# Optimization experiments

Measured on AMD Instinct MI355X. Metric: run time of the kernel, lower is better.

## Reference

```python
import jax, jax.numpy as jnp
import numpy as np

N = 50000      # nodes
E = 800000     # edges (avg degree 16)
F_IN = 128     # num_node_features
D = 64         # embedding_size (= per-head out_channels)
H = 4          # heads
ED = 20        # edge_dim (hardcoded in module)
SLOPE = 0.2    # GATv2 leaky_relu negative slope
N_LAYERS = 3   # conv applied 3 times with shared weights


def setup_inputs() -> dict:
    key = jax.random.key(0)
    ks = jax.random.split(key, 12)
    s = 0.1
    return {
        "x": jax.random.normal(ks[0], (N, F_IN), jnp.float32),
        "edge_attr": jax.random.normal(ks[1], (E, 2), jnp.float32),
        "edge_index": jax.random.randint(ks[2], (2, E), 0, N, dtype=jnp.int32),
        # f: Linear(F_IN, D)
        "f_W": jax.random.normal(ks[3], (F_IN, D), jnp.float32) * s,
        "f_b": jnp.zeros((D,), jnp.float32),
        # fe: Linear(2, ED)
        "fe_W": jax.random.normal(ks[4], (2, ED), jnp.float32) * s,
        "fe_b": jnp.zeros((ED,), jnp.float32),
        # GATv2Conv lin_l / lin_r: Linear(D, H*D)
        "Wl": jax.random.normal(ks[5], (D, H * D), jnp.float32) * s,
        "bl": jnp.zeros((H * D,), jnp.float32),
        "Wr": jax.random.normal(ks[6], (D, H * D), jnp.float32) * s,
        "br": jnp.zeros((H * D,), jnp.float32),
        # lin_edge: Linear(ED, H*D, bias=False)
        "We": jax.random.normal(ks[7], (ED, H * D), jnp.float32) * s,
        # attention vector att: [H, D]
        "att": jax.random.normal(ks[8], (H, D), jnp.float32) * s,
        # final bias (concat=False -> size D)
        "bias": jnp.zeros((D,), jnp.float32),
    }


def _gatv2_conv(h, e_emb, src, dst, Wl, bl, Wr, br, We, att, bias):
    # h: [N, D], e_emb: [E, ED], src/dst: [E]
    xl = (h @ Wl + bl).reshape(-1, H, D)        # source transform  [N,H,D]
    xr = (h @ Wr + br).reshape(-1, H, D)        # target transform  [N,H,D]
    ee = (e_emb @ We).reshape(-1, H, D)         # edge transform    [E,H,D]
    m = jax.nn.leaky_relu(xl[src] + xr[dst] + ee, SLOPE)  # [E,H,D]
    score = jnp.einsum('ehd,hd->eh', m, att)    # [E,H]
    # segment softmax over incoming edges of each dst node
    smax = jax.ops.segment_max(score, dst, num_segments=N)   # [N,H]
    ex = jnp.exp(score - smax[dst])
    denom = jax.ops.segment_sum(ex, dst, num_segments=N)     # [N,H]
    alpha = ex / denom[dst]                                  # [E,H]
    out = jax.ops.segment_sum(alpha[:, :, None] * xl[src], dst, num_segments=N)  # [N,H,D]
    return out.mean(axis=1) + bias              # concat=False -> head mean, [N,D]


def reference(x, edge_attr, edge_index, f_W, f_b, fe_W, fe_b, Wl, bl, Wr, br, We, att, bias):
    src, dst = edge_index[0], edge_index[1]
    h = jax.nn.relu(x @ f_W + f_b)
    e = jax.nn.relu(edge_attr @ fe_W + fe_b)
    for _ in range(N_LAYERS):
        h = jax.nn.relu(_gatv2_conv(h, e, src, dst, Wl, bl, Wr, br, We, att, bias))
    return h
```

## Files before the change

kernel.cpp:

```cpp
#include <hip/hip_runtime.h>
#include <math.h>

#define LN2_INV 1.4426950408889634f

__device__ __forceinline__ float fexp2(float x) {
#if __has_builtin(__builtin_amdgcn_exp2f)
    return __builtin_amdgcn_exp2f(x);
#else
    return exp2f(x);
#endif
}

__device__ __forceinline__ int rdlane_i(int v, int k) {
    return __builtin_amdgcn_readlane(v, k);
}

#define DPP_ADD4(P, CTRL)                                                                   \
    P.x += __int_as_float(__builtin_amdgcn_update_dpp(0, __float_as_int(P.x), CTRL, 0xf, 0xf, true)); \
    P.y += __int_as_float(__builtin_amdgcn_update_dpp(0, __float_as_int(P.y), CTRL, 0xf, 0xf, true)); \
    P.z += __int_as_float(__builtin_amdgcn_update_dpp(0, __float_as_int(P.z), CTRL, 0xf, 0xf, true)); \
    P.w += __int_as_float(__builtin_amdgcn_update_dpp(0, __float_as_int(P.w), CTRL, 0xf, 0xf, true));

__device__ __forceinline__ float4 wave_sum4(float4 p) {
    DPP_ADD4(p, 0x111)
    DPP_ADD4(p, 0x112)
    DPP_ADD4(p, 0x114)
    DPP_ADD4(p, 0x118)
    DPP_ADD4(p, 0x142)
    DPP_ADD4(p, 0x143)
    float4 r;
    r.x = __int_as_float(rdlane_i(__float_as_int(p.x), 63));
    r.y = __int_as_float(rdlane_i(__float_as_int(p.y), 63));
    r.z = __int_as_float(rdlane_i(__float_as_int(p.z), 63));
    r.w = __int_as_float(rdlane_i(__float_as_int(p.w), 63));
    return r;
}

__global__ void k_prep(const float* __restrict__ Wl, const float* __restrict__ Wr,
                       const float* __restrict__ We, const float* __restrict__ att,
                       float* __restrict__ Wlp, float* __restrict__ Wrp,
                       float* __restrict__ Wep, float* __restrict__ attp) {
    int t = blockIdx.x * 256 + threadIdx.x;
    if (t < 64 * 256) {
        int k = t >> 8, c = t & 255;
        int h = c >> 6, d = c & 63;
        int cp = d * 4 + h;
        Wlp[k * 256 + cp] = Wl[t];
        Wrp[k * 256 + cp] = Wr[t];
        if (k < 20) Wep[k * 256 + cp] = We[t];
        if (k == 0) {
            attp[cp] = att[c] * LN2_INV;
            attp[256 + cp] = 0.2f * att[c] * LN2_INV;
        }
    }
}

__global__ __launch_bounds__(256) void k_h0(const float* __restrict__ x,
                                            const float* __restrict__ fW,
                                            const float* __restrict__ fb,
                                            float* __restrict__ h0) {
    __shared__ __align__(16) float xs[8 * 128];
    int t = threadIdx.x;
    int base = blockIdx.x * 8;
#pragma unroll
    for (int r = 0; r < 4; ++r) { int j = r * 256 + t; xs[j] = x[base * 128 + j]; }
    __syncthreads();
    int c = t & 63, half = t >> 6;
    float acc0 = fb[c], acc1 = fb[c];
    int m0 = half, m1 = half + 4;
#pragma unroll 8
    for (int k0 = 0; k0 < 128; k0 += 4) {
        float4 a = *(const float4*)&xs[m0 * 128 + k0];
        float4 b = *(const float4*)&xs[m1 * 128 + k0];
        float w0 = fW[(k0 + 0) * 64 + c], w1 = fW[(k0 + 1) * 64 + c];
        float w2 = fW[(k0 + 2) * 64 + c], w3 = fW[(k0 + 3) * 64 + c];
        acc0 = fmaf(a.x, w0, fmaf(a.y, w1, fmaf(a.z, w2, fmaf(a.w, w3, acc0))));
        acc1 = fmaf(b.x, w0, fmaf(b.y, w1, fmaf(b.z, w2, fmaf(b.w, w3, acc1))));
    }
    h0[(base + m0) * 64 + c] = fmaxf(acc0, 0.f);
    h0[(base + m1) * 64 + c] = fmaxf(acc1, 0.f);
}

__global__ __launch_bounds__(256) void k_xlxr(const float* __restrict__ h,
                                              const float* __restrict__ Wlp,
                                              const float* __restrict__ Wrp,
                                              const float* __restrict__ bl,
                                              const float* __restrict__ br,
                                              float* __restrict__ xl,
                                              float* __restrict__ xr) {
    __shared__ __align__(16) float hs[16 * 64];
    int t = threadIdx.x;
    int base = blockIdx.x * 16;
#pragma unroll
    for (int r = 0; r < 4; ++r) hs[r * 256 + t] = h[base * 64 + r * 256 + t];
    __syncthreads();
    int hh = t & 3, d = t >> 2;
    int co = hh * 64 + d;
    float bL = bl[co], bR = br[co];
    float accl[16], accr[16];
#pragma unroll
    for (int m = 0; m < 16; ++m) { accl[m] = bL; accr[m] = bR; }
#pragma unroll 4
    for (int k0 = 0; k0 < 64; k0 += 4) {
        float wl[4], wr[4];
#pragma unroll
        for (int q = 0; q < 4; ++q) {
            wl[q] = Wlp[(k0 + q) * 256 + t];
            wr[q] = Wrp[(k0 + q) * 256 + t];
        }
#pragma unroll
        for (int m = 0; m < 16; ++m) {
            float4 hv = *(const float4*)&hs[m * 64 + k0];
            accl[m] = fmaf(hv.x, wl[0], fmaf(hv.y, wl[1], fmaf(hv.z, wl[2], fmaf(hv.w, wl[3], accl[m]))));
            accr[m] = fmaf(hv.x, wr[0], fmaf(hv.y, wr[1], fmaf(hv.z, wr[2], fmaf(hv.w, wr[3], accr[m]))));
        }
    }
#pragma unroll
    for (int m = 0; m < 16; ++m) {
        xl[(base + m) * 256 + t] = accl[m];
        xr[(base + m) * 256 + t] = accr[m];
    }
}

__global__ void k_zero(int* __restrict__ deg, int* __restrict__ counter, int Nn) {
    int i = blockIdx.x * 256 + threadIdx.x;
    if (i < Nn) deg[i] = 0;
    if (i == 0) *counter = 0;
}

__global__ void k_count(const int* __restrict__ dstArr, int* __restrict__ deg, int Ee) {
    int e = blockIdx.x * 256 + threadIdx.x;
    if (e < Ee) atomicAdd(&deg[dstArr[e]], 1);
}

__global__ void k_alloc(const int* __restrict__ deg, int* __restrict__ counter,
                        int* __restrict__ start, int* __restrict__ cursor, int Nn) {
    int n = blockIdx.x * 256 + threadIdx.x;
    if (n < Nn) {
        int d = deg[n];
        int b = atomicAdd(counter, d);
        start[n] = b;
        cursor[n] = b;
    }
}

__global__ void k_fill(const int* __restrict__ dstArr, const int* __restrict__ srcArr,
                       const float* __restrict__ eattr, int* __restrict__ cursor,
                       int* __restrict__ rec, int Ee) {
    int e = blockIdx.x * 256 + threadIdx.x;
    if (e < Ee) {
        int p = atomicAdd(&cursor[dstArr[e]], 1);
        int* r = rec + (size_t)p * 32;
        r[0] = srcArr[e];
        r[21] = __float_as_int(eattr[2 * e]);
        r[22] = __float_as_int(eattr[2 * e + 1]);
    }
}

__global__ void k_expand(const float* __restrict__ feW, const float* __restrict__ feb,
                         int* __restrict__ rec, int Ee) {
    int p = blockIdx.x * 8 + (threadIdx.x >> 5);
    int k = threadIdx.x & 31;
    if (p < Ee && k < 20) {
        int* r = rec + (size_t)p * 32;
        float a0 = __int_as_float(r[21]);
        float a1 = __int_as_float(r[22]);
        float s = fmaf(a0, feW[k], fmaf(a1, feW[20 + k], feb[k]));
        r[1 + k] = __float_as_int(fmaxf(s, 0.f));
    }
}

__global__ __launch_bounds__(256, 3) void k_edge(
    const float4* __restrict__ xl4p, const float4* __restrict__ xr4p,
    const float4* __restrict__ attboth, const float4* __restrict__ we4p,
    const int* __restrict__ rec,
    const int* __restrict__ start, const int* __restrict__ deg,
    const float* __restrict__ bias, float* __restrict__ hout, int Nn) {
    int lane = threadIdx.x & 63;
    int n = (int)((blockIdx.x * (unsigned)blockDim.x + threadIdx.x) >> 6);
    if (n >= Nn) return;

    float b = bias[lane];
    int dn = deg[n];
    if (dn == 0) { hout[(size_t)n * 64 + lane] = fmaxf(b, 0.f); return; }
    int s0 = start[n];

    float4 att4  = attboth[lane];
    float4 att02 = attboth[64 + lane];
    float4 xr4 = xr4p[(size_t)n * 64 + lane];
    float4 we[20];
#pragma unroll
    for (int k = 0; k < 20; ++k) we[k] = we4p[k * 64 + lane];

    const int* rp = rec + (size_t)s0 * 32 + (lane & 31);
    int rv0 = rp[0];
    int rv1 = rp[(dn > 1 ? 1 : 0) * 32];
    int src0 = rdlane_i(rv0, 0);
    float4 xl0 = xl4p[(size_t)src0 * 64 + lane];

    float4 acc = make_float4(0.f, 0.f, 0.f, 0.f);
    float4 l   = make_float4(0.f, 0.f, 0.f, 0.f);

    for (int i = 0; i < dn; ++i) {
        int i2 = (i + 2 < dn) ? (i + 2) : (dn - 1);
        int rv2 = rp[i2 * 32];
        int src1 = rdlane_i(rv1, 0);
        float4 xl1 = xl4p[(size_t)src1 * 64 + lane];

        float4 ee = make_float4(0.f, 0.f, 0.f, 0.f);
#pragma unroll
        for (int k = 0; k < 20; ++k) {
            float sk = __int_as_float(rdlane_i(rv0, 1 + k));
            ee.x = fmaf(sk, we[k].x, ee.x);
            ee.y = fmaf(sk, we[k].y, ee.y);
            ee.z = fmaf(sk, we[k].z, ee.z);
            ee.w = fmaf(sk, we[k].w, ee.w);
        }

        float4 p; float v;
        v = xl0.x + xr4.x + ee.x; p.x = fmaf(att4.x, fmaxf(v, 0.f), att02.x * fminf(v, 0.f));
        v = xl0.y + xr4.y + ee.y; p.y = fmaf(att4.y, fmaxf(v, 0.f), att02.y * fminf(v, 0.f));
        v = xl0.z + xr4.z + ee.z; p.z = fmaf(att4.z, fmaxf(v, 0.f), att02.z * fminf(v, 0.f));
        v = xl0.w + xr4.w + ee.w; p.w = fmaf(att4.w, fmaxf(v, 0.f), att02.w * fminf(v, 0.f));

        float4 sc = wave_sum4(p);
        float wx = fexp2(sc.x), wy = fexp2(sc.y), wz = fexp2(sc.z), ww = fexp2(sc.w);
        l.x += wx; l.y += wy; l.z += wz; l.w += ww;
        acc.x = fmaf(wx, xl0.x, acc.x);
        acc.y = fmaf(wy, xl0.y, acc.y);
        acc.z = fmaf(wz, xl0.z, acc.z);
        acc.w = fmaf(ww, xl0.w, acc.w);

        rv0 = rv1; rv1 = rv2; xl0 = xl1;
    }

    float res = 0.25f * (acc.x / l.x + acc.y / l.y + acc.z / l.z + acc.w / l.w) + b;
    hout[(size_t)n * 64 + lane] = fmaxf(res, 0.f);
}

extern "C" void kernel_launch(void* const* d_in, const int* in_sizes, int n_in,
                              void* d_out, int out_size, void* d_ws, size_t ws_size,
                              hipStream_t stream) {
    const float* x     = (const float*)d_in[0];
    const float* eattr = (const float*)d_in[1];
    const int*   eidx  = (const int*)d_in[2];
    const float* fW    = (const float*)d_in[3];
    const float* fb    = (const float*)d_in[4];
    const float* feW   = (const float*)d_in[5];
    const float* feb   = (const float*)d_in[6];
    const float* Wl    = (const float*)d_in[7];
    const float* bl    = (const float*)d_in[8];
    const float* Wr    = (const float*)d_in[9];
    const float* br    = (const float*)d_in[10];
    const float* We    = (const float*)d_in[11];
    const float* att   = (const float*)d_in[12];
    const float* bias  = (const float*)d_in[13];
    float* out = (float*)d_out;

    const int N = in_sizes[0] / 128;
    const int E = in_sizes[1] / 2;
    const int* srcArr = eidx;
    const int* dstArr = eidx + E;

    char* p = (char*)d_ws;
    auto alloc = [&](size_t bytes) -> char* {
        char* r = p;
        p += (bytes + 255) & ~(size_t)255;
        return r;
    };
    float* hA   = (float*)alloc((size_t)N * 64 * 4);
    float* hB   = (float*)alloc((size_t)N * 64 * 4);
    float* xl   = (float*)alloc((size_t)N * 256 * 4);
    float* xr   = (float*)alloc((size_t)N * 256 * 4);
    float* Wlp  = (float*)alloc(64 * 256 * 4);
    float* Wrp  = (float*)alloc(64 * 256 * 4);
    float* Wep  = (float*)alloc(20 * 256 * 4);
    float* attp = (float*)alloc(512 * 4);
    int* deg    = (int*)alloc((size_t)N * 4);
    int* start  = (int*)alloc((size_t)N * 4);
    int* cursor = (int*)alloc((size_t)N * 4);
    int* counter = (int*)alloc(256);
    int* rec    = (int*)alloc((size_t)E * 32 * 4);

    k_prep<<<64, 256, 0, stream>>>(Wl, Wr, We, att, Wlp, Wrp, Wep, attp);
    k_h0<<<N / 8, 256, 0, stream>>>(x, fW, fb, hA);
    k_zero<<<(N + 255) / 256, 256, 0, stream>>>(deg, counter, N);
    k_count<<<(E + 255) / 256, 256, 0, stream>>>(dstArr, deg, E);
    k_alloc<<<(N + 255) / 256, 256, 0, stream>>>(deg, counter, start, cursor, N);
    k_fill<<<(E + 255) / 256, 256, 0, stream>>>(dstArr, srcArr, eattr, cursor, rec, E);
    k_expand<<<(E + 7) / 8, 256, 0, stream>>>(feW, feb, rec, E);

    const float* hin = hA;
    for (int layer = 0; layer < 3; ++layer) {
        float* hout = (layer == 2) ? out : ((layer == 0) ? hB : hA);
        k_xlxr<<<N / 16, 256, 0, stream>>>(hin, Wlp, Wrp, bl, br, xl, xr);
        k_edge<<<(N * 64) / 256, 256, 0, stream>>>(
            (const float4*)xl, (const float4*)xr, (const float4*)attp,
            (const float4*)Wep, rec, start, deg, bias, hout, N);
        hin = hout;
    }
}
```

Before: 1.120 ms.

## Use head-major layout in edge kernel and fuse edge-embedding expansion into fill

Drops the weight permutation kernel and uses the original head-major layout, so each lane holds four d values of one head. The per-edge score reduction becomes a 16-lane DPP row reduction plus one bpermute instead of a full-wave reduction of four values, and the head mean is taken with cross-row shuffles at the end. Edge records shrink from 32 to 24 words, and the edge embedding is computed inside the fill kernel. Each lane now loads the 20 edge features directly with a double-buffered prefetch rather than broadcasting them via readlane. In exchange, every lane issues many more scalar loads per edge, and the math uses packed two-wide vectors.

```diff
diff --git a/kernel.cpp b/kernel.cpp
--- a/kernel.cpp
+++ b/kernel.cpp
@@ -1,5 +1,7 @@
 #include <hip/hip_runtime.h>
 #include <math.h>
+
+typedef float v2f __attribute__((ext_vector_type(2)));
 
 #define LN2_INV 1.4426950408889634f
 
@@ -11,49 +13,15 @@
 #endif
 }
 
-__device__ __forceinline__ int rdlane_i(int v, int k) {
-    return __builtin_amdgcn_readlane(v, k);
-}
-
-#define DPP_ADD4(P, CTRL)                                                                   \
-    P.x += __int_as_float(__builtin_amdgcn_update_dpp(0, __float_as_int(P.x), CTRL, 0xf, 0xf, true)); \
-    P.y += __int_as_float(__builtin_amdgcn_update_dpp(0, __float_as_int(P.y), CTRL, 0xf, 0xf, true)); \
-    P.z += __int_as_float(__builtin_amdgcn_update_dpp(0, __float_as_int(P.z), CTRL, 0xf, 0xf, true)); \
-    P.w += __int_as_float(__builtin_amdgcn_update_dpp(0, __float_as_int(P.w), CTRL, 0xf, 0xf, true));
-
-__device__ __forceinline__ float4 wave_sum4(float4 p) {
-    DPP_ADD4(p, 0x111)
-    DPP_ADD4(p, 0x112)
-    DPP_ADD4(p, 0x114)
-    DPP_ADD4(p, 0x118)
-    DPP_ADD4(p, 0x142)
-    DPP_ADD4(p, 0x143)
-    float4 r;
-    r.x = __int_as_float(rdlane_i(__float_as_int(p.x), 63));
-    r.y = __int_as_float(rdlane_i(__float_as_int(p.y), 63));
-    r.z = __int_as_float(rdlane_i(__float_as_int(p.z), 63));
-    r.w = __int_as_float(rdlane_i(__float_as_int(p.w), 63));
-    return r;
-}
-
-__global__ void k_prep(const float* __restrict__ Wl, const float* __restrict__ Wr,
-                       const float* __restrict__ We, const float* __restrict__ att,
-                       float* __restrict__ Wlp, float* __restrict__ Wrp,
-                       float* __restrict__ Wep, float* __restrict__ attp) {
-    int t = blockIdx.x * 256 + threadIdx.x;
-    if (t < 64 * 256) {
-        int k = t >> 8, c = t & 255;
-        int h = c >> 6, d = c & 63;
-        int cp = d * 4 + h;
-        Wlp[k * 256 + cp] = Wl[t];
-        Wrp[k * 256 + cp] = Wr[t];
-        if (k < 20) Wep[k * 256 + cp] = We[t];
-        if (k == 0) {
-            attp[cp] = att[c] * LN2_INV;
-            attp[256 + cp] = 0.2f * att[c] * LN2_INV;
-        }
-    }
-}
+__device__ __forceinline__ v2f max2(v2f a, float b) {
+    v2f r; r.x = fmaxf(a.x, b); r.y = fmaxf(a.y, b); return r;
+}
+__device__ __forceinline__ v2f min2(v2f a, float b) {
+    v2f r; r.x = fminf(a.x, b); r.y = fminf(a.y, b); return r;
+}
+
+#define DPP_ROW_ADD(V, CTRL) \
+    V += __int_as_float(__builtin_amdgcn_update_dpp(0, __float_as_int(V), CTRL, 0xf, 0xf, true));
 
 __global__ __launch_bounds__(256) void k_h0(const float* __restrict__ x,
                                             const float* __restrict__ fW,
@@ -82,8 +50,8 @@
 }
 
 __global__ __launch_bounds__(256) void k_xlxr(const float* __restrict__ h,
-                                              const float* __restrict__ Wlp,
-                                              const float* __restrict__ Wrp,
+                                              const float* __restrict__ Wl,
+                                              const float* __restrict__ Wr,
                                               const float* __restrict__ bl,
                                               const float* __restrict__ br,
                                               float* __restrict__ xl,
@@ -94,9 +62,7 @@
 #pragma unroll
     for (int r = 0; r < 4; ++r) hs[r * 256 + t] = h[base * 64 + r * 256 + t];
     __syncthreads();
-    int hh = t & 3, d = t >> 2;
-    int co = hh * 64 + d;
-    float bL = bl[co], bR = br[co];
+    float bL = bl[t], bR = br[t];
     float accl[16], accr[16];
 #pragma unroll
     for (int m = 0; m < 16; ++m) { accl[m] = bL; accr[m] = bR; }
@@ -105,8 +71,8 @@
         float wl[4], wr[4];
 #pragma unroll
         for (int q = 0; q < 4; ++q) {
-            wl[q] = Wlp[(k0 + q) * 256 + t];
-            wr[q] = Wrp[(k0 + q) * 256 + t];
+            wl[q] = Wl[(k0 + q) * 256 + t];
+            wr[q] = Wr[(k0 + q) * 256 + t];
         }
 #pragma unroll
         for (int m = 0; m < 16; ++m) {
@@ -145,97 +111,146 @@
 }
 
 __global__ void k_fill(const int* __restrict__ dstArr, const int* __restrict__ srcArr,
-                       const float* __restrict__ eattr, int* __restrict__ cursor,
+                       const float* __restrict__ eattr, const float* __restrict__ feW,
+                       const float* __restrict__ feb, int* __restrict__ cursor,
                        int* __restrict__ rec, int Ee) {
     int e = blockIdx.x * 256 + threadIdx.x;
-    if (e < Ee) {
-        int p = atomicAdd(&cursor[dstArr[e]], 1);
-        int* r = rec + (size_t)p * 32;
-        r[0] = srcArr[e];
-        r[21] = __float_as_int(eattr[2 * e]);
-        r[22] = __float_as_int(eattr[2 * e + 1]);
-    }
-}
-
-__global__ void k_expand(const float* __restrict__ feW, const float* __restrict__ feb,
-                         int* __restrict__ rec, int Ee) {
-    int p = blockIdx.x * 8 + (threadIdx.x >> 5);
-    int k = threadIdx.x & 31;
-    if (p < Ee && k < 20) {
-        int* r = rec + (size_t)p * 32;
-        float a0 = __int_as_float(r[21]);
-        float a1 = __int_as_float(r[22]);
-        float s = fmaf(a0, feW[k], fmaf(a1, feW[20 + k], feb[k]));
-        r[1 + k] = __float_as_int(fmaxf(s, 0.f));
-    }
+    if (e >= Ee) return;
+    float a0 = eattr[2 * e], a1 = eattr[2 * e + 1];
+    int p = atomicAdd(&cursor[dstArr[e]], 1);
+    float* r = (float*)(rec + (size_t)p * 24);
+    float s[20];
+#pragma unroll
+    for (int k = 0; k < 20; ++k)
+        s[k] = fmaxf(fmaf(a0, feW[k], fmaf(a1, feW[20 + k], feb[k])), 0.f);
+#pragma unroll
+    for (int j = 0; j < 5; ++j)
+        ((float4*)r)[j] = make_float4(s[4 * j], s[4 * j + 1], s[4 * j + 2], s[4 * j + 3]);
+    ((int*)r)[20] = srcArr[e];
 }
 
 __global__ __launch_bounds__(256, 3) void k_edge(
     const float4* __restrict__ xl4p, const float4* __restrict__ xr4p,
-    const float4* __restrict__ attboth, const float4* __restrict__ we4p,
-    const int* __restrict__ rec,
-    const int* __restrict__ start, const int* __restrict__ deg,
-    const float* __restrict__ bias, float* __restrict__ hout, int Nn) {
-    int lane = threadIdx.x & 63;
-    int n = (int)((blockIdx.x * (unsigned)blockDim.x + threadIdx.x) >> 6);
+    const float* __restrict__ att, const float4* __restrict__ We4,
+    const int* __restrict__ rec, const int* __restrict__ start,
+    const int* __restrict__ deg, const float* __restrict__ bias,
+    float* __restrict__ hout, int Nn) {
+    const int lane = threadIdx.x & 63;
+    const int n = (int)((blockIdx.x * 256u + threadIdx.x) >> 6);
     if (n >= Nn) return;
 
-    float b = bias[lane];
-    int dn = deg[n];
-    if (dn == 0) { hout[(size_t)n * 64 + lane] = fmaxf(b, 0.f); return; }
-    int s0 = start[n];
-
-    float4 att4  = attboth[lane];
-    float4 att02 = attboth[64 + lane];
-    float4 xr4 = xr4p[(size_t)n * 64 + lane];
-    float4 we[20];
-#pragma unroll
-    for (int k = 0; k < 20; ++k) we[k] = we4p[k * 64 + lane];
-
-    const int* rp = rec + (size_t)s0 * 32 + (lane & 31);
-    int rv0 = rp[0];
-    int rv1 = rp[(dn > 1 ? 1 : 0) * 32];
-    int src0 = rdlane_i(rv0, 0);
-    float4 xl0 = xl4p[(size_t)src0 * 64 + lane];
-
-    float4 acc = make_float4(0.f, 0.f, 0.f, 0.f);
-    float4 l   = make_float4(0.f, 0.f, 0.f, 0.f);
-
-    for (int i = 0; i < dn; ++i) {
-        int i2 = (i + 2 < dn) ? (i + 2) : (dn - 1);
-        int rv2 = rp[i2 * 32];
-        int src1 = rdlane_i(rv1, 0);
-        float4 xl1 = xl4p[(size_t)src1 * 64 + lane];
-
-        float4 ee = make_float4(0.f, 0.f, 0.f, 0.f);
-#pragma unroll
-        for (int k = 0; k < 20; ++k) {
-            float sk = __int_as_float(rdlane_i(rv0, 1 + k));
-            ee.x = fmaf(sk, we[k].x, ee.x);
-            ee.y = fmaf(sk, we[k].y, ee.y);
-            ee.z = fmaf(sk, we[k].z, ee.z);
-            ee.w = fmaf(sk, we[k].w, ee.w);
-        }
-
-        float4 p; float v;
-        v = xl0.x + xr4.x + ee.x; p.x = fmaf(att4.x, fmaxf(v, 0.f), att02.x * fminf(v, 0.f));
-        v = xl0.y + xr4.y + ee.y; p.y = fmaf(att4.y, fmaxf(v, 0.f), att02.y * fminf(v, 0.f));
-        v = xl0.z + xr4.z + ee.z; p.z = fmaf(att4.z, fmaxf(v, 0.f), att02.z * fminf(v, 0.f));
-        v = xl0.w + xr4.w + ee.w; p.w = fmaf(att4.w, fmaxf(v, 0.f), att02.w * fminf(v, 0.f));
-
-        float4 sc = wave_sum4(p);
-        float wx = fexp2(sc.x), wy = fexp2(sc.y), wz = fexp2(sc.z), ww = fexp2(sc.w);
-        l.x += wx; l.y += wy; l.z += wz; l.w += ww;
-        acc.x = fmaf(wx, xl0.x, acc.x);
-        acc.y = fmaf(wy, xl0.y, acc.y);
-        acc.z = fmaf(wz, xl0.z, acc.z);
-        acc.w = fmaf(ww, xl0.w, acc.w);
-
-        rv0 = rv1; rv1 = rv2; xl0 = xl1;
-    }
-
-    float res = 0.25f * (acc.x / l.x + acc.y / l.y + acc.z / l.z + acc.w / l.w) + b;
-    hout[(size_t)n * 64 + lane] = fmaxf(res, 0.f);
+    const int dn = __builtin_amdgcn_readfirstlane(deg[n]);
+    float4 bias4 = ((const float4*)bias)[lane & 15];
+    if (dn == 0) {
+        if (lane < 16) {
+            float4 o = make_float4(fmaxf(bias4.x, 0.f), fmaxf(bias4.y, 0.f),
+                                   fmaxf(bias4.z, 0.f), fmaxf(bias4.w, 0.f));
+            ((float4*)hout)[(size_t)n * 16 + lane] = o;
+        }
+        return;
+    }
+    const int s0 = __builtin_amdgcn_readfirstlane(start[n]);
+    const int* rb = rec + (size_t)s0 * 24;
+
+    float4 attv = ((const float4*)att)[lane];
+    v2f att01 = {attv.x * LN2_INV, attv.y * LN2_INV};
+    v2f att23 = {attv.z * LN2_INV, attv.w * LN2_INV};
+    v2f at201 = 0.2f * att01, at223 = 0.2f * att23;
+    float4 xrv = xr4p[(size_t)n * 64 + lane];
+    v2f xr01 = {xrv.x, xrv.y}, xr23 = {xrv.z, xrv.w};
+    v2f we01[20], we23[20];
+#pragma unroll
+    for (int k = 0; k < 20; ++k) {
+        float4 w = We4[k * 64 + lane];
+        we01[k].x = w.x; we01[k].y = w.y;
+        we23[k].x = w.z; we23[k].y = w.w;
+    }
+    const int bperm = ((lane & 48) | 15) << 2;
+
+    v2f acc01 = {0.f, 0.f}, acc23 = {0.f, 0.f};
+    float l = 0.f;
+
+    float sA[20], sB[20];
+    int src1, src2;
+
+#define LOADS(BUF, IDX)                                                     \
+    {                                                                       \
+        const int* q_ = rb + (size_t)(IDX) * 24;                            \
+        _Pragma("unroll")                                                   \
+        for (int k_ = 0; k_ < 20; ++k_) BUF[k_] = __int_as_float(q_[k_]);   \
+    }
+
+#define PROC(SBUF, XL)                                                      \
+    {                                                                       \
+        v2f xl01 = {XL.x, XL.y}, xl23 = {XL.z, XL.w};                       \
+        v2f ee01 = SBUF[0] * we01[0];                                       \
+        v2f ee23 = SBUF[0] * we23[0];                                       \
+        _Pragma("unroll")                                                   \
+        for (int k_ = 1; k_ < 20; ++k_) {                                   \
+            ee01 += SBUF[k_] * we01[k_];                                    \
+            ee23 += SBUF[k_] * we23[k_];                                    \
+        }                                                                   \
+        v2f v01 = xl01 + xr01 + ee01;                                       \
+        v2f v23 = xl23 + xr23 + ee23;                                       \
+        v2f p01 = att01 * max2(v01, 0.f) + at201 * min2(v01, 0.f);          \
+        v2f p23 = att23 * max2(v23, 0.f) + at223 * min2(v23, 0.f);          \
+        v2f pr = p01 + p23;                                                 \
+        float ps = pr.x + pr.y;                                             \
+        DPP_ROW_ADD(ps, 0x111)                                              \
+        DPP_ROW_ADD(ps, 0x112)                                              \
+        DPP_ROW_ADD(ps, 0x114)                                              \
+        DPP_ROW_ADD(ps, 0x118)                                              \
+        float sc = __int_as_float(                                          \
+            __builtin_amdgcn_ds_bpermute(bperm, __float_as_int(ps)));       \
+        float w_ = fexp2(sc);                                               \
+        l += w_;                                                            \
+        acc01 += w_ * xl01;                                                 \
+        acc23 += w_ * xl23;                                                 \
+    }
+
+    int i1 = dn > 1 ? 1 : 0;
+    LOADS(sA, 0)
+    int srcA0 = rb[20];
+    src1 = rb[(size_t)i1 * 24 + 20];
+    LOADS(sB, i1)
+    float4 xlA = xl4p[(size_t)srcA0 * 64 + lane];
+    float4 xlB;
+
+    int i = 0;
+    while (true) {
+        {
+            int ip2 = i + 2 < dn ? i + 2 : dn - 1;
+            src2 = rb[(size_t)ip2 * 24 + 20];
+            xlB = xl4p[(size_t)src1 * 64 + lane];
+            PROC(sA, xlA)
+            LOADS(sA, ip2)
+            src1 = src2;
+        }
+        if (++i >= dn) break;
+        {
+            int ip2 = i + 2 < dn ? i + 2 : dn - 1;
+            src2 = rb[(size_t)ip2 * 24 + 20];
+            xlA = xl4p[(size_t)src1 * 64 + lane];
+            PROC(sB, xlB)
+            LOADS(sB, ip2)
+            src1 = src2;
+        }
+        if (++i >= dn) break;
+    }
+
+    float inv = 0.25f / l;
+    float4 r = make_float4(acc01.x * inv, acc01.y * inv, acc23.x * inv, acc23.y * inv);
+    r.x += __shfl_xor(r.x, 16, 64); r.x += __shfl_xor(r.x, 32, 64);
+    r.y += __shfl_xor(r.y, 16, 64); r.y += __shfl_xor(r.y, 32, 64);
+    r.z += __shfl_xor(r.z, 16, 64); r.z += __shfl_xor(r.z, 32, 64);
+    r.w += __shfl_xor(r.w, 16, 64); r.w += __shfl_xor(r.w, 32, 64);
+    if (lane < 16) {
+        float4 o = make_float4(fmaxf(r.x + bias4.x, 0.f), fmaxf(r.y + bias4.y, 0.f),
+                               fmaxf(r.z + bias4.z, 0.f), fmaxf(r.w + bias4.w, 0.f));
+        ((float4*)hout)[(size_t)n * 16 + lane] = o;
+    }
+#undef LOADS
+#undef PROC
 }
 
 extern "C" void kernel_launch(void* const* d_in, const int* in_sizes, int n_in,
@@ -272,31 +287,26 @@
     float* hB   = (float*)alloc((size_t)N * 64 * 4);
     float* xl   = (float*)alloc((size_t)N * 256 * 4);
     float* xr   = (float*)alloc((size_t)N * 256 * 4);
-    float* Wlp  = (float*)alloc(64 * 256 * 4);
-    float* Wrp  = (float*)alloc(64 * 256 * 4);
-    float* Wep  = (float*)alloc(20 * 256 * 4);
-    float* attp = (float*)alloc(512 * 4);
     int* deg    = (int*)alloc((size_t)N * 4);
     int* start  = (int*)alloc((size_t)N * 4);
     int* cursor = (int*)alloc((size_t)N * 4);
     int* counter = (int*)alloc(256);
-    int* rec    = (int*)alloc((size_t)E * 32 * 4);
-
-    k_prep<<<64, 256, 0, stream>>>(Wl, Wr, We, att, Wlp, Wrp, Wep, attp);
+    int* rec    = (int*)alloc((size_t)E * 24 * 4);
+
     k_h0<<<N / 8, 256, 0, stream>>>(x, fW, fb, hA);
     k_zero<<<(N + 255) / 256, 256, 0, stream>>>(deg, counter, N);
     k_count<<<(E + 255) / 256, 256, 0, stream>>>(dstArr, deg, E);
     k_alloc<<<(N + 255) / 256, 256, 0, stream>>>(deg, counter, start, cursor, N);
-    k_fill<<<(E + 255) / 256, 256, 0, stream>>>(dstArr, srcArr, eattr, cursor, rec, E);
-    k_expand<<<(E + 7) / 8, 256, 0, stream>>>(feW, feb, rec, E);
+    k_fill<<<(E + 255) / 256, 256, 0, stream>>>(dstArr, srcArr, eattr, feW, feb,
+                                                cursor, rec, E);
 
     const float* hin = hA;
     for (int layer = 0; layer < 3; ++layer) {
         float* hout = (layer == 2) ? out : ((layer == 0) ? hB : hA);
-        k_xlxr<<<N / 16, 256, 0, stream>>>(hin, Wlp, Wrp, bl, br, xl, xr);
+        k_xlxr<<<N / 16, 256, 0, stream>>>(hin, Wl, Wr, bl, br, xl, xr);
         k_edge<<<(N * 64) / 256, 256, 0, stream>>>(
-            (const float4*)xl, (const float4*)xr, (const float4*)attp,
-            (const float4*)Wep, rec, start, deg, bias, hout, N);
+            (const float4*)xl, (const float4*)xr, att, (const float4*)We,
+            rec, start, deg, bias, hout, N);
         hin = hout;
     }
 }
```

Measured after the change: 1.745 ms. +55.7%, slower.
